# Kernel optimization log

Measured on AMD Instinct MI355X. Metric: run time of the kernel, lower is better.

## Reference

```python
import jax, jax.numpy as jnp
import numpy as np

EPS = 1e-6


def setup_inputs() -> dict:
    key = jax.random.key(0)
    k1, k2 = jax.random.split(key)
    x = jax.random.normal(k1, (4, 2048, 4096), dtype=jnp.float32)
    # module init: 0.01 * randn(n_reflections, n_features)
    vectors = 0.01 * jax.random.normal(k2, (16, 4096), dtype=jnp.float32)
    return {"x": x, "vectors": vectors}


def reference(x, vectors):
    """Apply k sequential Householder reflections: out <- out - 2 (out.v)/(v.v+eps) v."""
    orig_dtype = x.dtype
    out0 = x.astype(jnp.float32)
    vecs = vectors.astype(jnp.float32)

    def step(out, v):
        v_norm_sq = jnp.dot(v, v) + EPS            # scalar
        proj = jnp.einsum('...d,d->...', out, v)   # (B, L)
        out = out - (2.0 / v_norm_sq) * proj[..., None] * v
        return out, None

    out, _ = jax.lax.scan(step, out0, vecs)
    return out.astype(orig_dtype)
```

## Files before the change

### kernel.cpp

```cpp
#include <hip/hip_runtime.h>

#define HH_EPS 1e-6f


__global__ __launch_bounds__(256) void hh_gram(const float* __restrict__ V,
                                               float* __restrict__ ws) {
    int b = blockIdx.x;
    int k = 0;
    while (b >= k + 1) { b -= k + 1; ++k; }
    const int i = b;

    const float4* V4 = (const float4*)V;
    const int t = threadIdx.x;
    const int wave = t >> 6;
    const int lane = t & 63;

    float acc = 0.f;
    #pragma unroll
    for (int c = 0; c < 4; ++c) {
        const float4 a = V4[k * 1024 + t + 256 * c];
        const float4 v = V4[i * 1024 + t + 256 * c];
        acc = fmaf(a.x, v.x, acc);
        acc = fmaf(a.y, v.y, acc);
        acc = fmaf(a.z, v.z, acc);
        acc = fmaf(a.w, v.w, acc);
    }
    #pragma unroll
    for (int off = 32; off >= 1; off >>= 1)
        acc += __shfl_xor(acc, off, 64);

    __shared__ float red[4];
    if (lane == 0) red[wave] = acc;
    __syncthreads();
    if (t == 0) {
        const float g = red[0] + red[1] + red[2] + red[3];
        ws[k * 16 + i] = g;
        ws[i * 16 + k] = g;
    }
}

__global__ __launch_bounds__(64) void hh_T(float* __restrict__ ws) {
    __shared__ float Gs[256];
    const int t = threadIdx.x;
    #pragma unroll
    for (int q = 0; q < 4; ++q) Gs[t * 4 + q] = ws[t * 4 + q];
    __syncthreads();

    const int j = t;
    float tc[16];
    #pragma unroll
    for (int k = 0; k < 16; ++k) {
        const float beta = 2.0f / (Gs[k * 16 + k] + HH_EPS);
        float s = 0.f;
        #pragma unroll
        for (int i = 0; i < k; ++i) {
            const float g = Gs[k * 16 + i];
            s = fmaf((i >= j) ? g : 0.f, tc[i], s);
        }
        tc[k] = (j == k) ? beta : ((j < k) ? (-beta * s) : 0.f);
    }
    if (j < 16) {
        #pragma unroll
        for (int i = 0; i < 16; ++i) ws[256 + i * 16 + j] = tc[i];
    }
}

__global__ __launch_bounds__(256, 4) void hh_apply(const float* __restrict__ X,
                                                   const float* __restrict__ V,
                                                   const float* __restrict__ ws,
                                                   float* __restrict__ Out) {
    const float4* X4 = (const float4*)X;
    const float4* V4 = (const float4*)V;
    float4* O4 = (float4*)Out;

    const int t = threadIdx.x;
    const int wave = t >> 6;
    const int lane = t & 63;
    const int rb = blockIdx.x * 4;

    __shared__ float Ts[256];
    __shared__ float pw[16][4][4];
    __shared__ float yf[16][4];
    __shared__ float wf[16][4];

    float4 xr[4][4];
    #pragma unroll
    for (int r = 0; r < 4; ++r)
        #pragma unroll
        for (int c = 0; c < 4; ++c)
            xr[r][c] = X4[(rb + r) * 1024 + t + 256 * c];
    Ts[t] = ws[256 + t];

    for (int j = 0; j < 16; ++j) {
        float p0 = 0.f, p1 = 0.f, p2 = 0.f, p3 = 0.f;
        #pragma unroll
        for (int c = 0; c < 4; ++c) {
            const float4 b = V4[j * 1024 + t + 256 * c];
            p0 = fmaf(xr[0][c].x, b.x, p0); p0 = fmaf(xr[0][c].y, b.y, p0);
            p0 = fmaf(xr[0][c].z, b.z, p0); p0 = fmaf(xr[0][c].w, b.w, p0);
            p1 = fmaf(xr[1][c].x, b.x, p1); p1 = fmaf(xr[1][c].y, b.y, p1);
            p1 = fmaf(xr[1][c].z, b.z, p1); p1 = fmaf(xr[1][c].w, b.w, p1);
            p2 = fmaf(xr[2][c].x, b.x, p2); p2 = fmaf(xr[2][c].y, b.y, p2);
            p2 = fmaf(xr[2][c].z, b.z, p2); p2 = fmaf(xr[2][c].w, b.w, p2);
            p3 = fmaf(xr[3][c].x, b.x, p3); p3 = fmaf(xr[3][c].y, b.y, p3);
            p3 = fmaf(xr[3][c].z, b.z, p3); p3 = fmaf(xr[3][c].w, b.w, p3);
        }
        #pragma unroll
        for (int off = 32; off >= 1; off >>= 1) {
            p0 += __shfl_xor(p0, off, 64);
            p1 += __shfl_xor(p1, off, 64);
            p2 += __shfl_xor(p2, off, 64);
            p3 += __shfl_xor(p3, off, 64);
        }
        if (lane == 0) {
            pw[j][wave][0] = p0; pw[j][wave][1] = p1;
            pw[j][wave][2] = p2; pw[j][wave][3] = p3;
        }
    }
    __syncthreads();

    if (t < 64) {
        const int j = t >> 2, r = t & 3;
        yf[j][r] = pw[j][0][r] + pw[j][1][r] + pw[j][2][r] + pw[j][3][r];
    }
    __syncthreads();

    if (t < 64) {
        const int k = t >> 2, r = t & 3;
        float s = 0.f;
        #pragma unroll
        for (int j = 0; j < 16; ++j) s = fmaf(Ts[k * 16 + j], yf[j][r], s);
        wf[k][r] = s;
    }
    __syncthreads();

    for (int j = 0; j < 16; ++j) {
        const float w0 = -wf[j][0], w1 = -wf[j][1];
        const float w2 = -wf[j][2], w3 = -wf[j][3];
        #pragma unroll
        for (int c = 0; c < 4; ++c) {
            const float4 v = V4[j * 1024 + t + 256 * c];
            xr[0][c].x = fmaf(w0, v.x, xr[0][c].x);
            xr[0][c].y = fmaf(w0, v.y, xr[0][c].y);
            xr[0][c].z = fmaf(w0, v.z, xr[0][c].z);
            xr[0][c].w = fmaf(w0, v.w, xr[0][c].w);
            xr[1][c].x = fmaf(w1, v.x, xr[1][c].x);
            xr[1][c].y = fmaf(w1, v.y, xr[1][c].y);
            xr[1][c].z = fmaf(w1, v.z, xr[1][c].z);
            xr[1][c].w = fmaf(w1, v.w, xr[1][c].w);
            xr[2][c].x = fmaf(w2, v.x, xr[2][c].x);
            xr[2][c].y = fmaf(w2, v.y, xr[2][c].y);
            xr[2][c].z = fmaf(w2, v.z, xr[2][c].z);
            xr[2][c].w = fmaf(w2, v.w, xr[2][c].w);
            xr[3][c].x = fmaf(w3, v.x, xr[3][c].x);
            xr[3][c].y = fmaf(w3, v.y, xr[3][c].y);
            xr[3][c].z = fmaf(w3, v.z, xr[3][c].z);
            xr[3][c].w = fmaf(w3, v.w, xr[3][c].w);
        }
    }

    #pragma unroll
    for (int r = 0; r < 4; ++r)
        #pragma unroll
        for (int c = 0; c < 4; ++c)
            O4[(rb + r) * 1024 + t + 256 * c] = xr[r][c];
}

extern "C" void kernel_launch(void* const* d_in, const int* in_sizes, int n_in,
                              void* d_out, int out_size, void* d_ws, size_t ws_size,
                              hipStream_t stream) {
    const float* X = (const float*)d_in[0];
    const float* V = (const float*)d_in[1];
    float* O = (float*)d_out;
    float* ws = (float*)d_ws;

    hh_gram<<<136, 256, 0, stream>>>(V, ws);
    hh_T<<<1, 64, 0, stream>>>(ws);
    hh_apply<<<2048, 256, 0, stream>>>(X, V, ws, O);
}
```

Measured before the change: 290.8 us.

## Split Householder apply into separate projection, w-vector, and update kernels

Replaces the fused per-row-block apply kernel with three stages. A column-split projection kernel accumulates X·V^T into a workspace with atomics, a small kernel multiplies by T to form w, and an update kernel applies X - w V. This aims to remove the in-block shuffle reductions and serial per-reflection reduction latency. In exchange, X is read twice, the projection loads are strided across lanes, and atomics and extra launches are added.

```diff
diff --git a/kernel.cpp b/kernel.cpp
--- a/kernel.cpp
+++ b/kernel.cpp
@@ -2,6 +2,12 @@
 
 #define HH_EPS 1e-6f
 
+#define WS_YACC 512
+#define WS_WBUF (512 + 131072)
+
+__global__ __launch_bounds__(256) void hh_zero_y(float* __restrict__ ws) {
+    ws[WS_YACC + blockIdx.x * 256 + threadIdx.x] = 0.f;
+}
 
 __global__ __launch_bounds__(256) void hh_gram(const float* __restrict__ V,
                                                float* __restrict__ ws) {
@@ -65,78 +71,102 @@
     }
 }
 
-__global__ __launch_bounds__(256, 4) void hh_apply(const float* __restrict__ X,
-                                                   const float* __restrict__ V,
-                                                   const float* __restrict__ ws,
-                                                   float* __restrict__ Out) {
+__global__ __launch_bounds__(256) void hh_project(const float* __restrict__ X,
+                                                  const float* __restrict__ V,
+                                                  float* __restrict__ ws) {
+    const int rg = blockIdx.x >> 4;
+    const int cs = blockIdx.x & 15;
+    const int wave = threadIdx.x >> 6;
+    const int lane = threadIdx.x & 63;
+    const int row = rg * 256 + wave * 64 + lane;
+
+    const float4* X4 = (const float4*)X + (size_t)row * 1024 + cs * 64;
+    const float4* V4 = (const float4*)V + cs * 64;
+
+    float acc[16];
+    #pragma unroll
+    for (int j = 0; j < 16; ++j) acc[j] = 0.f;
+
+    for (int it = 0; it < 16; ++it) {
+        float4 xq[4];
+        #pragma unroll
+        for (int q = 0; q < 4; ++q) xq[q] = X4[it * 4 + q];
+        #pragma unroll
+        for (int q = 0; q < 4; ++q) {
+            #pragma unroll
+            for (int j = 0; j < 16; ++j) {
+                const float4 v = V4[j * 1024 + it * 4 + q];
+                float s = acc[j];
+                s = fmaf(xq[q].x, v.x, s);
+                s = fmaf(xq[q].y, v.y, s);
+                s = fmaf(xq[q].z, v.z, s);
+                s = fmaf(xq[q].w, v.w, s);
+                acc[j] = s;
+            }
+        }
+    }
+
+    float* yacc = ws + WS_YACC + (size_t)row * 16;
+    #pragma unroll
+    for (int j = 0; j < 16; ++j) atomicAdd(&yacc[j], acc[j]);
+}
+
+__global__ __launch_bounds__(256) void hh_wvec(float* __restrict__ ws) {
+    __shared__ float Ts[256];
+    Ts[threadIdx.x] = ws[256 + threadIdx.x];
+    __syncthreads();
+
+    const int r = blockIdx.x * 256 + threadIdx.x;
+    const float4* y4 = (const float4*)(ws + WS_YACC) + (size_t)r * 4;
+    float y[16];
+    #pragma unroll
+    for (int q = 0; q < 4; ++q) {
+        const float4 v = y4[q];
+        y[q * 4 + 0] = v.x; y[q * 4 + 1] = v.y;
+        y[q * 4 + 2] = v.z; y[q * 4 + 3] = v.w;
+    }
+    float4* w4 = (float4*)(ws + WS_WBUF) + (size_t)r * 4;
+    #pragma unroll
+    for (int q = 0; q < 4; ++q) {
+        float4 o;
+        float* op = (float*)&o;
+        #pragma unroll
+        for (int kk = 0; kk < 4; ++kk) {
+            const int k = q * 4 + kk;
+            float s = 0.f;
+            #pragma unroll
+            for (int j = 0; j < 16; ++j) s = fmaf(Ts[k * 16 + j], y[j], s);
+            op[kk] = s;
+        }
+        w4[q] = o;
+    }
+}
+
+__global__ __launch_bounds__(256) void hh_update(const float* __restrict__ X,
+                                                 const float* __restrict__ V,
+                                                 const float* __restrict__ ws,
+                                                 float* __restrict__ Out) {
     const float4* X4 = (const float4*)X;
     const float4* V4 = (const float4*)V;
     float4* O4 = (float4*)Out;
 
     const int t = threadIdx.x;
-    const int wave = t >> 6;
-    const int lane = t & 63;
     const int rb = blockIdx.x * 4;
 
-    __shared__ float Ts[256];
-    __shared__ float pw[16][4][4];
-    __shared__ float yf[16][4];
-    __shared__ float wf[16][4];
+    __shared__ float wf[4][16];
+    if (t < 64) wf[t >> 4][t & 15] = ws[WS_WBUF + rb * 16 + t];
 
     float4 xr[4][4];
     #pragma unroll
     for (int r = 0; r < 4; ++r)
         #pragma unroll
         for (int c = 0; c < 4; ++c)
-            xr[r][c] = X4[(rb + r) * 1024 + t + 256 * c];
-    Ts[t] = ws[256 + t];
+            xr[r][c] = X4[(size_t)(rb + r) * 1024 + t + 256 * c];
+    __syncthreads();
 
     for (int j = 0; j < 16; ++j) {
-        float p0 = 0.f, p1 = 0.f, p2 = 0.f, p3 = 0.f;
-        #pragma unroll
-        for (int c = 0; c < 4; ++c) {
-            const float4 b = V4[j * 1024 + t + 256 * c];
-            p0 = fmaf(xr[0][c].x, b.x, p0); p0 = fmaf(xr[0][c].y, b.y, p0);
-            p0 = fmaf(xr[0][c].z, b.z, p0); p0 = fmaf(xr[0][c].w, b.w, p0);
-            p1 = fmaf(xr[1][c].x, b.x, p1); p1 = fmaf(xr[1][c].y, b.y, p1);
-            p1 = fmaf(xr[1][c].z, b.z, p1); p1 = fmaf(xr[1][c].w, b.w, p1);
-            p2 = fmaf(xr[2][c].x, b.x, p2); p2 = fmaf(xr[2][c].y, b.y, p2);
-            p2 = fmaf(xr[2][c].z, b.z, p2); p2 = fmaf(xr[2][c].w, b.w, p2);
-            p3 = fmaf(xr[3][c].x, b.x, p3); p3 = fmaf(xr[3][c].y, b.y, p3);
-            p3 = fmaf(xr[3][c].z, b.z, p3); p3 = fmaf(xr[3][c].w, b.w, p3);
-        }
-        #pragma unroll
-        for (int off = 32; off >= 1; off >>= 1) {
-            p0 += __shfl_xor(p0, off, 64);
-            p1 += __shfl_xor(p1, off, 64);
-            p2 += __shfl_xor(p2, off, 64);
-            p3 += __shfl_xor(p3, off, 64);
-        }
-        if (lane == 0) {
-            pw[j][wave][0] = p0; pw[j][wave][1] = p1;
-            pw[j][wave][2] = p2; pw[j][wave][3] = p3;
-        }
-    }
-    __syncthreads();
-
-    if (t < 64) {
-        const int j = t >> 2, r = t & 3;
-        yf[j][r] = pw[j][0][r] + pw[j][1][r] + pw[j][2][r] + pw[j][3][r];
-    }
-    __syncthreads();
-
-    if (t < 64) {
-        const int k = t >> 2, r = t & 3;
-        float s = 0.f;
-        #pragma unroll
-        for (int j = 0; j < 16; ++j) s = fmaf(Ts[k * 16 + j], yf[j][r], s);
-        wf[k][r] = s;
-    }
-    __syncthreads();
-
-    for (int j = 0; j < 16; ++j) {
-        const float w0 = -wf[j][0], w1 = -wf[j][1];
-        const float w2 = -wf[j][2], w3 = -wf[j][3];
+        const float w0 = -wf[0][j], w1 = -wf[1][j];
+        const float w2 = -wf[2][j], w3 = -wf[3][j];
         #pragma unroll
         for (int c = 0; c < 4; ++c) {
             const float4 v = V4[j * 1024 + t + 256 * c];
@@ -163,7 +193,7 @@
     for (int r = 0; r < 4; ++r)
         #pragma unroll
         for (int c = 0; c < 4; ++c)
-            O4[(rb + r) * 1024 + t + 256 * c] = xr[r][c];
+            O4[(size_t)(rb + r) * 1024 + t + 256 * c] = xr[r][c];
 }
 
 extern "C" void kernel_launch(void* const* d_in, const int* in_sizes, int n_in,
@@ -174,7 +204,10 @@
     float* O = (float*)d_out;
     float* ws = (float*)d_ws;
 
+    hh_zero_y<<<512, 256, 0, stream>>>(ws);
     hh_gram<<<136, 256, 0, stream>>>(V, ws);
     hh_T<<<1, 64, 0, stream>>>(ws);
-    hh_apply<<<2048, 256, 0, stream>>>(X, V, ws, O);
-}
+    hh_project<<<512, 256, 0, stream>>>(X, V, ws);
+    hh_wvec<<<32, 256, 0, stream>>>(ws);
+    hh_update<<<2048, 256, 0, stream>>>(X, V, ws, O);
+}
```

Measured after the change: 417.5 us. 43.6% more time.

## Precompute V^T T product so apply kernel skips in-block T multiply

Applied to the files above, without the earlier changes.

Adds a small kernel that forms B = T^T V (16x4096) once in the workspace, so the apply kernel uses the raw projections y directly with B instead of computing w = T y per block with extra shared-memory barriers. The projection phase is also restructured to load four reflection vectors at a time with batched shuffle reductions, and the update loop is partially unrolled. This removes one barrier and the per-block T multiply, at the cost of an extra launch and reading B instead of V in the update phase.

```diff
diff --git a/kernel.cpp b/kernel.cpp
--- a/kernel.cpp
+++ b/kernel.cpp
@@ -65,12 +65,33 @@
     }
 }
 
+__global__ __launch_bounds__(256) void hh_B2(const float* __restrict__ V,
+                                             float* __restrict__ ws) {
+    const float* T = ws + 256;
+    float4* B4 = (float4*)(ws + 512);
+    const float4* V4 = (const float4*)V;
+    const int tid = blockIdx.x * 256 + threadIdx.x;
+    const int j = tid >> 10;
+    const int d4 = tid & 1023;
+    float4 acc = make_float4(0.f, 0.f, 0.f, 0.f);
+    for (int k = j; k < 16; ++k) {
+        const float tv = T[k * 16 + j];
+        const float4 v = V4[k * 1024 + d4];
+        acc.x = fmaf(tv, v.x, acc.x);
+        acc.y = fmaf(tv, v.y, acc.y);
+        acc.z = fmaf(tv, v.z, acc.z);
+        acc.w = fmaf(tv, v.w, acc.w);
+    }
+    B4[tid] = acc;
+}
+
 __global__ __launch_bounds__(256, 4) void hh_apply(const float* __restrict__ X,
                                                    const float* __restrict__ V,
                                                    const float* __restrict__ ws,
                                                    float* __restrict__ Out) {
     const float4* X4 = (const float4*)X;
     const float4* V4 = (const float4*)V;
+    const float4* B24 = (const float4*)(ws + 512);
     float4* O4 = (float4*)Out;
 
     const int t = threadIdx.x;
@@ -78,84 +99,91 @@
     const int lane = t & 63;
     const int rb = blockIdx.x * 4;
 
-    __shared__ float Ts[256];
-    __shared__ float pw[16][4][4];
-    __shared__ float yf[16][4];
-    __shared__ float wf[16][4];
+    __shared__ alignas(16) float pw[4][16][4];
+    __shared__ alignas(16) float yw[16][4];
 
     float4 xr[4][4];
     #pragma unroll
     for (int r = 0; r < 4; ++r)
         #pragma unroll
         for (int c = 0; c < 4; ++c)
-            xr[r][c] = X4[(rb + r) * 1024 + t + 256 * c];
-    Ts[t] = ws[256 + t];
-
-    for (int j = 0; j < 16; ++j) {
-        float p0 = 0.f, p1 = 0.f, p2 = 0.f, p3 = 0.f;
+            xr[r][c] = X4[(size_t)(rb + r) * 1024 + t + 256 * c];
+
+    #pragma unroll
+    for (int g = 0; g < 4; ++g) {
+        float acc[4][4];
+        #pragma unroll
+        for (int jj = 0; jj < 4; ++jj)
+            #pragma unroll
+            for (int r = 0; r < 4; ++r) acc[jj][r] = 0.f;
+
         #pragma unroll
         for (int c = 0; c < 4; ++c) {
-            const float4 b = V4[j * 1024 + t + 256 * c];
-            p0 = fmaf(xr[0][c].x, b.x, p0); p0 = fmaf(xr[0][c].y, b.y, p0);
-            p0 = fmaf(xr[0][c].z, b.z, p0); p0 = fmaf(xr[0][c].w, b.w, p0);
-            p1 = fmaf(xr[1][c].x, b.x, p1); p1 = fmaf(xr[1][c].y, b.y, p1);
-            p1 = fmaf(xr[1][c].z, b.z, p1); p1 = fmaf(xr[1][c].w, b.w, p1);
-            p2 = fmaf(xr[2][c].x, b.x, p2); p2 = fmaf(xr[2][c].y, b.y, p2);
-            p2 = fmaf(xr[2][c].z, b.z, p2); p2 = fmaf(xr[2][c].w, b.w, p2);
-            p3 = fmaf(xr[3][c].x, b.x, p3); p3 = fmaf(xr[3][c].y, b.y, p3);
-            p3 = fmaf(xr[3][c].z, b.z, p3); p3 = fmaf(xr[3][c].w, b.w, p3);
-        }
+            float4 bv[4];
+            #pragma unroll
+            for (int jj = 0; jj < 4; ++jj)
+                bv[jj] = V4[(4 * g + jj) * 1024 + t + 256 * c];
+            #pragma unroll
+            for (int jj = 0; jj < 4; ++jj) {
+                #pragma unroll
+                for (int r = 0; r < 4; ++r) {
+                    float s = acc[jj][r];
+                    s = fmaf(xr[r][c].x, bv[jj].x, s);
+                    s = fmaf(xr[r][c].y, bv[jj].y, s);
+                    s = fmaf(xr[r][c].z, bv[jj].z, s);
+                    s = fmaf(xr[r][c].w, bv[jj].w, s);
+                    acc[jj][r] = s;
+                }
+            }
+        }
+
         #pragma unroll
         for (int off = 32; off >= 1; off >>= 1) {
-            p0 += __shfl_xor(p0, off, 64);
-            p1 += __shfl_xor(p1, off, 64);
-            p2 += __shfl_xor(p2, off, 64);
-            p3 += __shfl_xor(p3, off, 64);
-        }
+            #pragma unroll
+            for (int jj = 0; jj < 4; ++jj)
+                #pragma unroll
+                for (int r = 0; r < 4; ++r)
+                    acc[jj][r] += __shfl_xor(acc[jj][r], off, 64);
+        }
+
         if (lane == 0) {
-            pw[j][wave][0] = p0; pw[j][wave][1] = p1;
-            pw[j][wave][2] = p2; pw[j][wave][3] = p3;
+            #pragma unroll
+            for (int jj = 0; jj < 4; ++jj)
+                *(float4*)&pw[wave][4 * g + jj][0] =
+                    make_float4(acc[jj][0], acc[jj][1], acc[jj][2], acc[jj][3]);
         }
     }
     __syncthreads();
 
     if (t < 64) {
         const int j = t >> 2, r = t & 3;
-        yf[j][r] = pw[j][0][r] + pw[j][1][r] + pw[j][2][r] + pw[j][3][r];
-    }
-    __syncthreads();
-
-    if (t < 64) {
-        const int k = t >> 2, r = t & 3;
-        float s = 0.f;
-        #pragma unroll
-        for (int j = 0; j < 16; ++j) s = fmaf(Ts[k * 16 + j], yf[j][r], s);
-        wf[k][r] = s;
-    }
-    __syncthreads();
-
+        yw[j][r] = pw[0][j][r] + pw[1][j][r] + pw[2][j][r] + pw[3][j][r];
+    }
+    __syncthreads();
+
+    #pragma unroll 2
     for (int j = 0; j < 16; ++j) {
-        const float w0 = -wf[j][0], w1 = -wf[j][1];
-        const float w2 = -wf[j][2], w3 = -wf[j][3];
+        const float4 y4 = *(const float4*)&yw[j][0];
+        const float n0 = -y4.x, n1 = -y4.y, n2 = -y4.z, n3 = -y4.w;
         #pragma unroll
         for (int c = 0; c < 4; ++c) {
-            const float4 v = V4[j * 1024 + t + 256 * c];
-            xr[0][c].x = fmaf(w0, v.x, xr[0][c].x);
-            xr[0][c].y = fmaf(w0, v.y, xr[0][c].y);
-            xr[0][c].z = fmaf(w0, v.z, xr[0][c].z);
-            xr[0][c].w = fmaf(w0, v.w, xr[0][c].w);
-            xr[1][c].x = fmaf(w1, v.x, xr[1][c].x);
-            xr[1][c].y = fmaf(w1, v.y, xr[1][c].y);
-            xr[1][c].z = fmaf(w1, v.z, xr[1][c].z);
-            xr[1][c].w = fmaf(w1, v.w, xr[1][c].w);
-            xr[2][c].x = fmaf(w2, v.x, xr[2][c].x);
-            xr[2][c].y = fmaf(w2, v.y, xr[2][c].y);
-            xr[2][c].z = fmaf(w2, v.z, xr[2][c].z);
-            xr[2][c].w = fmaf(w2, v.w, xr[2][c].w);
-            xr[3][c].x = fmaf(w3, v.x, xr[3][c].x);
-            xr[3][c].y = fmaf(w3, v.y, xr[3][c].y);
-            xr[3][c].z = fmaf(w3, v.z, xr[3][c].z);
-            xr[3][c].w = fmaf(w3, v.w, xr[3][c].w);
+            const float4 b = B24[j * 1024 + t + 256 * c];
+            xr[0][c].x = fmaf(n0, b.x, xr[0][c].x);
+            xr[0][c].y = fmaf(n0, b.y, xr[0][c].y);
+            xr[0][c].z = fmaf(n0, b.z, xr[0][c].z);
+            xr[0][c].w = fmaf(n0, b.w, xr[0][c].w);
+            xr[1][c].x = fmaf(n1, b.x, xr[1][c].x);
+            xr[1][c].y = fmaf(n1, b.y, xr[1][c].y);
+            xr[1][c].z = fmaf(n1, b.z, xr[1][c].z);
+            xr[1][c].w = fmaf(n1, b.w, xr[1][c].w);
+            xr[2][c].x = fmaf(n2, b.x, xr[2][c].x);
+            xr[2][c].y = fmaf(n2, b.y, xr[2][c].y);
+            xr[2][c].z = fmaf(n2, b.z, xr[2][c].z);
+            xr[2][c].w = fmaf(n2, b.w, xr[2][c].w);
+            xr[3][c].x = fmaf(n3, b.x, xr[3][c].x);
+            xr[3][c].y = fmaf(n3, b.y, xr[3][c].y);
+            xr[3][c].z = fmaf(n3, b.z, xr[3][c].z);
+            xr[3][c].w = fmaf(n3, b.w, xr[3][c].w);
         }
     }
 
@@ -163,7 +191,7 @@
     for (int r = 0; r < 4; ++r)
         #pragma unroll
         for (int c = 0; c < 4; ++c)
-            O4[(rb + r) * 1024 + t + 256 * c] = xr[r][c];
+            O4[(size_t)(rb + r) * 1024 + t + 256 * c] = xr[r][c];
 }
 
 extern "C" void kernel_launch(void* const* d_in, const int* in_sizes, int n_in,
@@ -176,5 +204,6 @@
 
     hh_gram<<<136, 256, 0, stream>>>(V, ws);
     hh_T<<<1, 64, 0, stream>>>(ws);
+    hh_B2<<<64, 256, 0, stream>>>(V, ws);
     hh_apply<<<2048, 256, 0, stream>>>(X, V, ws, O);
 }
```

Result: slower. 405.2 us (+39.3%).
